# Kernel optimization log

Hardware: AMD Instinct MI355X
Metric: run time of the kernel (lower is better)

Reference implementation:

```python
import jax, jax.numpy as jnp
import numpy as np

B, IN, OUT = 131072, 256, 256
BITWIDTH = 7.0


def setup_inputs() -> dict:
    key = jax.random.key(0)
    k1, k2 = jax.random.split(key)
    # simulated int8 activations (integer-valued float32)
    act_in = jax.random.randint(k1, (B, IN), -127, 128).astype(jnp.float32)
    # UniformWeights: xavier_uniform then weight_quant to the int8 grid
    limit = float(np.sqrt(6.0 / (IN + OUT)))
    w = jax.random.uniform(k2, (OUT, IN), minval=-limit, maxval=limit, dtype=jnp.float32)
    w_range = jnp.max(jnp.abs(w))
    weight_exp = (jnp.ceil(jnp.log2(w_range)) - 7.0).astype(jnp.int32)
    weight = jnp.round(w / w_range * 127.0)  # int8-valued float32 [OUT, IN]
    return {"act_in": act_in, "exp_in": jnp.int32(0), "weight": weight, "weight_exp": weight_exp}


def _round_shift(x, shift):
    # RoundShift: floor-div by 2**shift, add floor(|remainder| / 2**(shift-1)), clip to int8
    two_s = jnp.exp2(shift)
    rt = jnp.floor(x / two_s)
    prob = jnp.abs(x - rt * two_s)
    dec = jnp.floor(prob / jnp.exp2(shift - 1.0))
    return jnp.clip(rt + dec, -127.0, 127.0)


def reference(act_in, exp_in, weight, weight_exp):
    # int8 GEMM simulated in fp32 (exact: |acc| < 2^24)
    temp = act_in @ weight.T  # [B, OUT] int32 accumulator values
    # RangeEstimate: full-tensor abs-max -> bitwidth
    r = jnp.max(jnp.abs(temp))
    bw = jnp.where(r > 0, jnp.ceil(jnp.log2(jnp.maximum(r, 1.0))), 0.0)
    shift = bw - BITWIDTH
    pos = shift > 0
    safe_shift = jnp.maximum(shift, 1.0)
    rounded = _round_shift(temp, safe_shift)
    act_out = jnp.where(pos, rounded, temp).astype(jnp.int8)
    exp_sum = jnp.asarray(exp_in, jnp.int32) + jnp.asarray(weight_exp, jnp.int32)
    exp_out = (exp_sum + jnp.where(pos, shift, 0.0).astype(jnp.int32)).astype(jnp.int16)
    return act_out, exp_out
```

## Files before the change

kernel.cpp:

```cpp
#include <hip/hip_runtime.h>
#include <stdint.h>


#define M_ROWS 131072
#define NK 256
#define BM 256
#define BST 264

typedef __attribute__((ext_vector_type(8))) short bf16x8;
typedef __attribute__((ext_vector_type(4))) float f32x4;
typedef __attribute__((ext_vector_type(4))) float fv4;
typedef __attribute__((ext_vector_type(4))) int iv4;
typedef __attribute__((ext_vector_type(4))) unsigned int u32x4;
typedef __attribute__((ext_vector_type(4))) unsigned short us4;

__device__ __forceinline__ uint32_t pack_bf16(float a, float b) {
  return __builtin_amdgcn_perm(__float_as_uint(b), __float_as_uint(a),
                               0x07060302u);
}

__global__ void wconv(const float* __restrict__ w, unsigned short* __restrict__ wb,
                      int* __restrict__ gmax) {
  if (blockIdx.x == 0 && threadIdx.x == 0) *gmax = 0;
  const int i = blockIdx.x * 256 + threadIdx.x;
  const fv4 f = ((const fv4*)w)[i];
  us4 o;
  o.x = (unsigned short)(__float_as_uint(f.x) >> 16);
  o.y = (unsigned short)(__float_as_uint(f.y) >> 16);
  o.z = (unsigned short)(__float_as_uint(f.z) >> 16);
  o.w = (unsigned short)(__float_as_uint(f.w) >> 16);
  ((us4*)wb)[i] = o;
}

__global__ __launch_bounds__(1024, 4) void gemm_maxstore(
    const float* __restrict__ act, const unsigned short* __restrict__ wgtb,
    int* __restrict__ out, int* __restrict__ gmax)
{
  __shared__ __align__(16) short Bs[NK * BST];
  __shared__ int smax;
  const int tid = threadIdx.x;
  if (tid == 0) smax = 0;

  for (int c = tid; c < NK * NK / 8; c += 1024) {
    const int col = c >> 5;
    const int k8  = (c & 31) << 3;
    *(u32x4*)&Bs[col * BST + k8] = ((const u32x4*)wgtb)[c];
  }
  __syncthreads();

  const int lane = tid & 63;
  const int wave = tid >> 6;
  const int wr   = wave >> 2;
  const int wc   = wave & 3;
  const int lm   = lane & 15;
  const int lk   = lane >> 4;
  const int bm   = blockIdx.x * BM;

  const float* abase = act + (size_t)(bm + wr * 64 + lm) * NK + lk * 8;

  f32x4 acc[4][4] = {};
#pragma unroll
  for (int kk = 0; kk < 8; ++kk) {
    bf16x8 bfr[4];
#pragma unroll
    for (int ni = 0; ni < 4; ++ni)
      bfr[ni] = *(const bf16x8*)
          &Bs[(wc * 64 + ni * 16 + lm) * BST + kk * 32 + lk * 8];
#pragma unroll
    for (int mi = 0; mi < 4; ++mi) {
      const float* p = abase + (size_t)(mi * 16) * NK + kk * 32;
      const fv4 f0 = *(const fv4*)p;
      const fv4 f1 = *((const fv4*)p + 1);
      u32x4 apk;
      apk.x = pack_bf16(f0.x, f0.y); apk.y = pack_bf16(f0.z, f0.w);
      apk.z = pack_bf16(f1.x, f1.y); apk.w = pack_bf16(f1.z, f1.w);
      const bf16x8 af = __builtin_bit_cast(bf16x8, apk);
#pragma unroll
      for (int ni = 0; ni < 4; ++ni)
        acc[mi][ni] = __builtin_amdgcn_mfma_f32_16x16x32_bf16(
            af, bfr[ni], acc[mi][ni], 0, 0, 0);
    }
  }

  int imax = 0;
#pragma unroll
  for (int mi = 0; mi < 4; ++mi)
#pragma unroll
    for (int ni = 0; ni < 4; ++ni)
#pragma unroll
      for (int r = 0; r < 4; ++r) {
        const int ti = (int)acc[mi][ni][r];
        const int a = ti < 0 ? -ti : ti;
        imax = a > imax ? a : imax;
        const int m = bm + wr * 64 + mi * 16 + lk * 4 + r;
        const int n = wc * 64 + ni * 16 + lm;
        out[(size_t)m * NK + n] = ti;
      }
#pragma unroll
  for (int off = 32; off; off >>= 1) {
    const int o = __shfl_xor(imax, off, 64);
    imax = o > imax ? o : imax;
  }
  if (lane == 0) atomicMax(&smax, imax);
  __syncthreads();
  if (tid == 0) atomicMax(gmax, smax);
}

__global__ __launch_bounds__(256) void quant_pass(
    int* __restrict__ out, const int* __restrict__ gmax,
    const int* __restrict__ exp_in, const int* __restrict__ wexp)
{
  const int rmax = *gmax;
  const int bw = (rmax <= 1) ? 0 : (32 - __clz(rmax - 1));
  const int shift = bw - 7;
  const bool pos = shift > 0;
  const int s = shift < 1 ? 1 : shift;

  const size_t total  = (size_t)M_ROWS * NK / 4;
  const size_t stride = (size_t)gridDim.x * blockDim.x;
  for (size_t i = (size_t)blockIdx.x * blockDim.x + threadIdx.x; i < total;
       i += stride) {
    iv4 t = ((const iv4*)out)[i];
    iv4 q;
#pragma unroll
    for (int j = 0; j < 4; ++j) {
      const int ti = t[j];
      int r;
      if (pos) {
        const int rt = ti >> s;
        const int dec = (ti - (rt << s)) >> (s - 1);
        r = rt + dec;
        r = r > 127 ? 127 : (r < -127 ? -127 : r);
      } else {
        r = (int)(signed char)(ti & 0xFF);
      }
      q[j] = r;
    }
    __builtin_nontemporal_store(q, &((iv4*)out)[i]);
  }

  if (blockIdx.x == 0 && threadIdx.x == 0) {
    const int e = exp_in[0] + wexp[0] + (pos ? shift : 0);
    out[(size_t)M_ROWS * NK] = (int)(short)e;
  }
}

extern "C" void kernel_launch(void* const* d_in, const int* in_sizes, int n_in,
                              void* d_out, int out_size, void* d_ws, size_t ws_size,
                              hipStream_t stream) {
  const float* act   = (const float*)d_in[0];
  const int* exp_in  = (const int*)d_in[1];
  const float* wgt   = (const float*)d_in[2];
  const int* wexp    = (const int*)d_in[3];
  int* gmax          = (int*)d_ws;
  unsigned short* wb = (unsigned short*)((char*)d_ws + 128);

  wconv<<<dim3(64), dim3(256), 0, stream>>>(wgt, wb, gmax);
  gemm_maxstore<<<dim3(M_ROWS / BM), dim3(1024), 0, stream>>>(act, wb, (int*)d_out,
                                                              gmax);
  quant_pass<<<dim3(2048), dim3(256), 0, stream>>>((int*)d_out, gmax, exp_in, wexp);
}
```

Before: 293.2 us.

## Recompute int8 GEMM in two passes instead of storing and requantizing int32 accumulators

Replaces the bf16 MFMA GEMM with int8 MFMA (v_mfma_i32_16x16x64_i8) on activations packed to int8. The first pass converts activations to int8, writes them to workspace, and computes only the global abs-max. The second pass redoes the GEMM from the int8 copy and quantizes in the epilogue. This removes the int32 intermediate round trip through d_out (a 128MB write plus read) at the cost of doing the GEMM twice and adding a 32MB int8 activation buffer. Occupancy drops to one 512-thread block per CU, and a global grid sync is still needed between the two kernels.

New measurement: 267.6 us. 8.7% less time.

```diff
diff --git a/kernel.cpp b/kernel.cpp
--- a/kernel.cpp
+++ b/kernel.cpp
@@ -4,49 +4,47 @@
 
 #define M_ROWS 131072
 #define NK 256
-#define BM 256
-#define BST 264
-
-typedef __attribute__((ext_vector_type(8))) short bf16x8;
-typedef __attribute__((ext_vector_type(4))) float f32x4;
+#define TM 128
+#define TILES 4
+#define LSTR 272
+
+typedef __attribute__((ext_vector_type(4))) int iv4;
 typedef __attribute__((ext_vector_type(4))) float fv4;
-typedef __attribute__((ext_vector_type(4))) int iv4;
 typedef __attribute__((ext_vector_type(4))) unsigned int u32x4;
-typedef __attribute__((ext_vector_type(4))) unsigned short us4;
-
-__device__ __forceinline__ uint32_t pack_bf16(float a, float b) {
-  return __builtin_amdgcn_perm(__float_as_uint(b), __float_as_uint(a),
-                               0x07060302u);
-}
-
-__global__ void wconv(const float* __restrict__ w, unsigned short* __restrict__ wb,
+
+__device__ __forceinline__ iv4 mfma_i8(iv4 a, iv4 b, iv4 c) {
+  asm("v_mfma_i32_16x16x64_i8 %0, %1, %2, %0" : "+v"(c) : "v"(a), "v"(b));
+  return c;
+}
+
+__device__ __forceinline__ unsigned int pack_i8x4(float a, float b, float c,
+                                                  float d) {
+  return ((unsigned int)(int)a & 0xFFu) | (((unsigned int)(int)b & 0xFFu) << 8) |
+         (((unsigned int)(int)c & 0xFFu) << 16) | ((unsigned int)(int)d << 24);
+}
+
+__global__ void wconv(const float* __restrict__ w, unsigned char* __restrict__ wi8,
                       int* __restrict__ gmax) {
   if (blockIdx.x == 0 && threadIdx.x == 0) *gmax = 0;
   const int i = blockIdx.x * 256 + threadIdx.x;
   const fv4 f = ((const fv4*)w)[i];
-  us4 o;
-  o.x = (unsigned short)(__float_as_uint(f.x) >> 16);
-  o.y = (unsigned short)(__float_as_uint(f.y) >> 16);
-  o.z = (unsigned short)(__float_as_uint(f.z) >> 16);
-  o.w = (unsigned short)(__float_as_uint(f.w) >> 16);
-  ((us4*)wb)[i] = o;
-}
-
-__global__ __launch_bounds__(1024, 4) void gemm_maxstore(
-    const float* __restrict__ act, const unsigned short* __restrict__ wgtb,
-    int* __restrict__ out, int* __restrict__ gmax)
+  ((unsigned int*)wi8)[i] = pack_i8x4(f.x, f.y, f.z, f.w);
+}
+
+__global__ __launch_bounds__(512, 1) void gemm_max_cvt(
+    const float* __restrict__ act, const unsigned char* __restrict__ wi8,
+    unsigned char* __restrict__ act8, int* __restrict__ gmax)
 {
-  __shared__ __align__(16) short Bs[NK * BST];
+  __shared__ __align__(16) unsigned char As[TM * LSTR];
+  __shared__ __align__(16) unsigned char Bs[NK * LSTR];
   __shared__ int smax;
   const int tid = threadIdx.x;
   if (tid == 0) smax = 0;
 
-  for (int c = tid; c < NK * NK / 8; c += 1024) {
-    const int col = c >> 5;
-    const int k8  = (c & 31) << 3;
-    *(u32x4*)&Bs[col * BST + k8] = ((const u32x4*)wgtb)[c];
-  }
-  __syncthreads();
+  for (int c = tid; c < NK * NK / 16; c += 512) {
+    const int col = c >> 4, kc = (c & 15) << 4;
+    *(u32x4*)&Bs[col * LSTR + kc] = *(const u32x4*)(wi8 + col * NK + kc);
+  }
 
   const int lane = tid & 63;
   const int wave = tid >> 6;
@@ -54,48 +52,62 @@
   const int wc   = wave & 3;
   const int lm   = lane & 15;
   const int lk   = lane >> 4;
-  const int bm   = blockIdx.x * BM;
-
-  const float* abase = act + (size_t)(bm + wr * 64 + lm) * NK + lk * 8;
-
-  f32x4 acc[4][4] = {};
-#pragma unroll
-  for (int kk = 0; kk < 8; ++kk) {
-    bf16x8 bfr[4];
-#pragma unroll
-    for (int ni = 0; ni < 4; ++ni)
-      bfr[ni] = *(const bf16x8*)
-          &Bs[(wc * 64 + ni * 16 + lm) * BST + kk * 32 + lk * 8];
-#pragma unroll
-    for (int mi = 0; mi < 4; ++mi) {
-      const float* p = abase + (size_t)(mi * 16) * NK + kk * 32;
-      const fv4 f0 = *(const fv4*)p;
-      const fv4 f1 = *((const fv4*)p + 1);
-      u32x4 apk;
-      apk.x = pack_bf16(f0.x, f0.y); apk.y = pack_bf16(f0.z, f0.w);
-      apk.z = pack_bf16(f1.x, f1.y); apk.w = pack_bf16(f1.z, f1.w);
-      const bf16x8 af = __builtin_bit_cast(bf16x8, apk);
-#pragma unroll
-      for (int ni = 0; ni < 4; ++ni)
-        acc[mi][ni] = __builtin_amdgcn_mfma_f32_16x16x32_bf16(
-            af, bfr[ni], acc[mi][ni], 0, 0, 0);
-    }
-  }
 
   int imax = 0;
-#pragma unroll
-  for (int mi = 0; mi < 4; ++mi)
-#pragma unroll
-    for (int ni = 0; ni < 4; ++ni)
-#pragma unroll
-      for (int r = 0; r < 4; ++r) {
-        const int ti = (int)acc[mi][ni][r];
-        const int a = ti < 0 ? -ti : ti;
-        imax = a > imax ? a : imax;
-        const int m = bm + wr * 64 + mi * 16 + lk * 4 + r;
-        const int n = wc * 64 + ni * 16 + lm;
-        out[(size_t)m * NK + n] = ti;
-      }
+
+  for (int t = 0; t < TILES; ++t) {
+    const int tb = blockIdx.x * (TILES * TM) + t * TM;
+
+    __syncthreads();
+#pragma unroll
+    for (int j = 0; j < 4; ++j) {
+      const int c   = j * 512 + tid;
+      const int row = c >> 4;
+      const int kc  = (c & 15) << 4;
+      const float* p = act + (size_t)(tb + row) * NK + kc;
+      const fv4 f0 = ((const fv4*)p)[0];
+      const fv4 f1 = ((const fv4*)p)[1];
+      const fv4 f2 = ((const fv4*)p)[2];
+      const fv4 f3 = ((const fv4*)p)[3];
+      u32x4 v;
+      v.x = pack_i8x4(f0.x, f0.y, f0.z, f0.w);
+      v.y = pack_i8x4(f1.x, f1.y, f1.z, f1.w);
+      v.z = pack_i8x4(f2.x, f2.y, f2.z, f2.w);
+      v.w = pack_i8x4(f3.x, f3.y, f3.z, f3.w);
+      *(u32x4*)&As[row * LSTR + kc] = v;
+      *(u32x4*)(act8 + (size_t)(tb + row) * NK + kc) = v;
+    }
+    __syncthreads();
+
+    iv4 acc[4][4] = {};
+#pragma unroll
+    for (int kk = 0; kk < 4; ++kk) {
+      iv4 af[4], bf[4];
+#pragma unroll
+      for (int mi = 0; mi < 4; ++mi)
+        af[mi] = *(const iv4*)&As[(wr * 64 + mi * 16 + lm) * LSTR + kk * 64 + lk * 16];
+#pragma unroll
+      for (int ni = 0; ni < 4; ++ni)
+        bf[ni] = *(const iv4*)&Bs[(wc * 64 + ni * 16 + lm) * LSTR + kk * 64 + lk * 16];
+#pragma unroll
+      for (int mi = 0; mi < 4; ++mi)
+#pragma unroll
+        for (int ni = 0; ni < 4; ++ni)
+          acc[mi][ni] = mfma_i8(af[mi], bf[ni], acc[mi][ni]);
+    }
+
+#pragma unroll
+    for (int mi = 0; mi < 4; ++mi)
+#pragma unroll
+      for (int ni = 0; ni < 4; ++ni)
+#pragma unroll
+        for (int r = 0; r < 4; ++r) {
+          const int ti = acc[mi][ni][r];
+          const int a = ti < 0 ? -ti : ti;
+          imax = a > imax ? a : imax;
+        }
+  }
+
 #pragma unroll
   for (int off = 32; off; off >>= 1) {
     const int o = __shfl_xor(imax, off, 64);
@@ -106,40 +118,87 @@
   if (tid == 0) atomicMax(gmax, smax);
 }
 
-__global__ __launch_bounds__(256) void quant_pass(
+__global__ __launch_bounds__(512, 1) void gemm_quant(
+    const unsigned char* __restrict__ act8, const unsigned char* __restrict__ wi8,
     int* __restrict__ out, const int* __restrict__ gmax,
     const int* __restrict__ exp_in, const int* __restrict__ wexp)
 {
+  __shared__ __align__(16) unsigned char As[TM * LSTR];
+  __shared__ __align__(16) unsigned char Bs[NK * LSTR];
+
   const int rmax = *gmax;
   const int bw = (rmax <= 1) ? 0 : (32 - __clz(rmax - 1));
   const int shift = bw - 7;
   const bool pos = shift > 0;
   const int s = shift < 1 ? 1 : shift;
 
-  const size_t total  = (size_t)M_ROWS * NK / 4;
-  const size_t stride = (size_t)gridDim.x * blockDim.x;
-  for (size_t i = (size_t)blockIdx.x * blockDim.x + threadIdx.x; i < total;
-       i += stride) {
-    iv4 t = ((const iv4*)out)[i];
-    iv4 q;
+  const int tid = threadIdx.x;
+  for (int c = tid; c < NK * NK / 16; c += 512) {
+    const int col = c >> 4, kc = (c & 15) << 4;
+    *(u32x4*)&Bs[col * LSTR + kc] = *(const u32x4*)(wi8 + col * NK + kc);
+  }
+
+  const int lane = tid & 63;
+  const int wave = tid >> 6;
+  const int wr   = wave >> 2;
+  const int wc   = wave & 3;
+  const int lm   = lane & 15;
+  const int lk   = lane >> 4;
+
+  for (int t = 0; t < TILES; ++t) {
+    const int tb = blockIdx.x * (TILES * TM) + t * TM;
+
+    __syncthreads();
 #pragma unroll
     for (int j = 0; j < 4; ++j) {
-      const int ti = t[j];
-      int r;
-      if (pos) {
-        const int rt = ti >> s;
-        const int dec = (ti - (rt << s)) >> (s - 1);
-        r = rt + dec;
-        r = r > 127 ? 127 : (r < -127 ? -127 : r);
-      } else {
-        r = (int)(signed char)(ti & 0xFF);
-      }
-      q[j] = r;
-    }
-    __builtin_nontemporal_store(q, &((iv4*)out)[i]);
-  }
-
-  if (blockIdx.x == 0 && threadIdx.x == 0) {
+      const int c   = j * 512 + tid;
+      const int row = c >> 4;
+      const int kc  = (c & 15) << 4;
+      *(u32x4*)&As[row * LSTR + kc] =
+          *(const u32x4*)(act8 + (size_t)(tb + row) * NK + kc);
+    }
+    __syncthreads();
+
+    iv4 acc[4][4] = {};
+#pragma unroll
+    for (int kk = 0; kk < 4; ++kk) {
+      iv4 af[4], bf[4];
+#pragma unroll
+      for (int mi = 0; mi < 4; ++mi)
+        af[mi] = *(const iv4*)&As[(wr * 64 + mi * 16 + lm) * LSTR + kk * 64 + lk * 16];
+#pragma unroll
+      for (int ni = 0; ni < 4; ++ni)
+        bf[ni] = *(const iv4*)&Bs[(wc * 64 + ni * 16 + lm) * LSTR + kk * 64 + lk * 16];
+#pragma unroll
+      for (int mi = 0; mi < 4; ++mi)
+#pragma unroll
+        for (int ni = 0; ni < 4; ++ni)
+          acc[mi][ni] = mfma_i8(af[mi], bf[ni], acc[mi][ni]);
+    }
+
+#pragma unroll
+    for (int mi = 0; mi < 4; ++mi)
+#pragma unroll
+      for (int ni = 0; ni < 4; ++ni)
+#pragma unroll
+        for (int r = 0; r < 4; ++r) {
+          const int ti = acc[mi][ni][r];
+          int q;
+          if (pos) {
+            const int rt = ti >> s;
+            const int dec = (ti - (rt << s)) >> (s - 1);
+            q = rt + dec;
+            q = q > 127 ? 127 : (q < -127 ? -127 : q);
+          } else {
+            q = (int)(signed char)(ti & 0xFF);
+          }
+          const int m = tb + wr * 64 + mi * 16 + lk * 4 + r;
+          const int n = wc * 64 + ni * 16 + lm;
+          __builtin_nontemporal_store(q, &out[(size_t)m * NK + n]);
+        }
+  }
+
+  if (blockIdx.x == 0 && tid == 0) {
     const int e = exp_in[0] + wexp[0] + (pos ? shift : 0);
     out[(size_t)M_ROWS * NK] = (int)(short)e;
   }
@@ -152,11 +211,13 @@
   const int* exp_in  = (const int*)d_in[1];
   const float* wgt   = (const float*)d_in[2];
   const int* wexp    = (const int*)d_in[3];
-  int* gmax          = (int*)d_ws;
-  unsigned short* wb = (unsigned short*)((char*)d_ws + 128);
-
-  wconv<<<dim3(64), dim3(256), 0, stream>>>(wgt, wb, gmax);
-  gemm_maxstore<<<dim3(M_ROWS / BM), dim3(1024), 0, stream>>>(act, wb, (int*)d_out,
-                                                              gmax);
-  quant_pass<<<dim3(2048), dim3(256), 0, stream>>>((int*)d_out, gmax, exp_in, wexp);
-}
+  int* gmax           = (int*)d_ws;
+  unsigned char* wi8  = (unsigned char*)d_ws + 4096;
+  unsigned char* act8 = (unsigned char*)d_ws + (1 << 20);
+
+  wconv<<<dim3(64), dim3(256), 0, stream>>>(wgt, wi8, gmax);
+  gemm_max_cvt<<<dim3(M_ROWS / (TILES * TM)), dim3(512), 0, stream>>>(
+      act, wi8, act8, gmax);
+  gemm_quant<<<dim3(M_ROWS / (TILES * TM)), dim3(512), 0, stream>>>(
+      act8, wi8, (int*)d_out, gmax, exp_in, wexp);
+}
```
